# Optimization experiments

Hardware: AMD Instinct MI355X
Metric: run time of the kernel (lower is better)

## Reference

```python
import jax, jax.numpy as jnp
import numpy as np

B, C, H, W = 8, 384, 32, 32
HEADS = 12


def _relative_position_index(h, w):
    coords_h = np.arange(h)
    coords_w = np.arange(w)
    coords = np.stack(np.meshgrid(coords_h, coords_w, indexing='ij'))  # [2,h,w]
    flat = coords.reshape(2, -1)  # [2, N]
    rel = flat[:, :, None] - flat[:, None, :]  # [2, N, N]
    rel = rel.transpose(1, 2, 0)  # [N, N, 2]
    rel[:, :, 0] += h - 1
    rel[:, :, 1] += w - 1
    rel[:, :, 0] *= 2 * w - 1
    return rel.sum(-1).astype(np.int32)  # [N, N]


def setup_inputs() -> dict:
    key = jax.random.key(0)
    ks = jax.random.split(key, 6)
    std = 0.02
    x = jax.random.normal(ks[0], (B, C, H, W), dtype=jnp.float32)
    q_w = jax.random.normal(ks[1], (C, C), dtype=jnp.float32) * std
    q_b = jnp.zeros((C,), dtype=jnp.float32)
    kv_w = jax.random.normal(ks[2], (2 * C, C), dtype=jnp.float32) * std
    kv_b = jnp.zeros((2 * C,), dtype=jnp.float32)
    proj_w = jax.random.normal(ks[3], (C, C), dtype=jnp.float32) * std
    proj_b = jnp.zeros((C,), dtype=jnp.float32)
    n_table = (2 * H - 1) * (2 * W - 1)
    rpb_table = jax.random.normal(ks[4], (n_table, HEADS), dtype=jnp.float32) * std
    rel_index = jnp.asarray(_relative_position_index(H, W))  # [N, N] int32
    return {"x": x, "q_w": q_w, "q_b": q_b, "kv_w": kv_w, "kv_b": kv_b,
            "proj_w": proj_w, "proj_b": proj_b, "rpb_table": rpb_table,
            "rel_index": rel_index}


def reference(x, q_w, q_b, kv_w, kv_b, proj_w, proj_b, rpb_table, rel_index):
    b, c, h, w = x.shape
    n = h * w
    heads = rpb_table.shape[-1]
    hd = c // heads
    scale = hd ** (-0.5)

    xf = x.reshape(b, c, n)  # 1x1 conv == per-pixel matmul
    q = jnp.einsum('dc,bcn->bdn', q_w, xf) + q_b[:, None]
    q = q.reshape(b, heads, hd, n).transpose(0, 1, 3, 2)  # [b,h,n,hd]
    kv = jnp.einsum('dc,bcn->bdn', kv_w, xf) + kv_b[:, None]
    kv = kv.reshape(b, 2, heads, hd, n)
    k = kv[:, 0].transpose(0, 1, 3, 2)  # [b,h,n,hd]
    v = kv[:, 1].transpose(0, 1, 3, 2)

    attn = jnp.einsum('bhnd,bhmd->bhnm', q, k) * scale  # [b,h,n,n]
    bias = rpb_table[rel_index.reshape(-1)].reshape(n, n, heads)
    bias = bias.transpose(2, 0, 1)  # [h,n,n]
    attn = jax.nn.softmax(attn + bias[None], axis=-1)

    out = jnp.einsum('bhnm,bhmd->bhnd', attn, v)
    out = out.transpose(0, 1, 3, 2).reshape(b, c, h, w)
    out = jnp.einsum('dc,bchw->bdhw', proj_w, out) + proj_b[None, :, None, None]
    return out
```

## Files before the change

### kernel.cpp

```cpp
#include <hip/hip_runtime.h>
#include <hip/hip_bf16.h>

#define B_  8
#define C_  384
#define N_  1024
#define NH_ 12
#define HD_ 32
#define D3_ 1152

typedef __bf16 bf16x8 __attribute__((ext_vector_type(8)));
typedef __bf16 bf16x2 __attribute__((ext_vector_type(2)));
typedef float  f32x4  __attribute__((ext_vector_type(4)));

typedef const __attribute__((address_space(1))) unsigned int guint;
typedef __attribute__((address_space(3))) unsigned int luint;

__device__ __forceinline__ float b2f(ushort u) {
    return __uint_as_float(((unsigned int)u) << 16);
}
__device__ __forceinline__ ushort f2b(float f) {
    unsigned int i = __float_as_uint(f);
    unsigned int r = i + 0x7fffu + ((i >> 16) & 1u);
    return (ushort)(r >> 16);
}
__device__ __forceinline__ unsigned pk2(float a, float b) {
#if __has_builtin(__builtin_amdgcn_cvt_pk_bf16_f32)
    bf16x2 t = __builtin_amdgcn_cvt_pk_bf16_f32(a, b);
    return __builtin_bit_cast(unsigned, t);
#else
    return (unsigned)f2b(a) | ((unsigned)f2b(b) << 16);
#endif
}

#if __has_builtin(__builtin_amdgcn_exp2f)
#define EXP2 __builtin_amdgcn_exp2f
#else
#define EXP2 exp2f
#endif

__device__ __forceinline__ void gl2lds16(const void* g, void* l) {
    __builtin_amdgcn_global_load_lds((guint*)g, (luint*)l, 16, 0, 0);
}

#define C1_ 0.25505654204433796f
#define C2_ 1.4426950408889634f
#define TS_ 3972

__global__ __launch_bounds__(256) void setup(
    const float* __restrict__ x, const float* __restrict__ q_w,
    const float* __restrict__ kv_w, const float* __restrict__ proj_w,
    const float* __restrict__ q_b, const float* __restrict__ kv_b,
    const float* __restrict__ tab,
    ushort* __restrict__ xT, float* __restrict__ tabT,
    ushort* __restrict__ Wall, ushort* __restrict__ PW,
    float* __restrict__ ballf)
{
    __shared__ ushort T[64 * 72];
    const int bx = blockIdx.x, tid = threadIdx.x;

    if (bx < 768) {
        int t = bx;
        int nx = t & 15, cy = (t >> 4) % 6, b = t / 96;
        int n0 = nx * 64, c0 = cy * 64;
        {
            int i = tid >> 2;
            int ns = (tid & 3) * 16;
            const float* src = x + ((size_t)b * C_ + c0 + i) * N_ + n0 + ns;
            #pragma unroll
            for (int k4 = 0; k4 < 4; ++k4) {
                float4 f = *(const float4*)(src + k4 * 4);
                T[(ns + k4 * 4 + 0) * 72 + i] = f2b(f.x);
                T[(ns + k4 * 4 + 1) * 72 + i] = f2b(f.y);
                T[(ns + k4 * 4 + 2) * 72 + i] = f2b(f.z);
                T[(ns + k4 * 4 + 3) * 72 + i] = f2b(f.w);
            }
        }
        __syncthreads();
        {
            int j = tid >> 2;
            int cs = (tid & 3) * 16;
            ushort* dst = xT + ((size_t)b * N_ + n0 + j) * C_ + c0 + cs;
            *(uint4*)dst       = *(const uint4*)&T[j * 72 + cs];
            *(uint4*)(dst + 8) = *(const uint4*)&T[j * 72 + cs + 8];
        }
    } else if (bx < 1346) {
        const int NW4 = 110592, NP4 = 36864, NB4 = 288;
        int t = (bx - 768) * 256 + tid;
        if (t < NW4) {
            int e = t * 4;
            float4 f = (e < 147456) ? *(const float4*)(q_w + e)
                                    : *(const float4*)(kv_w + e - 147456);
            union { uint2 u; ushort s[4]; } o;
            o.u.x = pk2(f.x, f.y); o.u.y = pk2(f.z, f.w);
            *(uint2*)(Wall + e) = o.u;
        } else if (t < NW4 + NP4) {
            int e = (t - NW4) * 4;
            float4 f = *(const float4*)(proj_w + e);
            union { uint2 u; ushort s[4]; } o;
            o.u.x = pk2(f.x, f.y); o.u.y = pk2(f.z, f.w);
            *(uint2*)(PW + e) = o.u;
        } else if (t < NW4 + NP4 + NB4) {
            int e = (t - NW4 - NP4) * 4;
            float4 f = (e < 384) ? *(const float4*)(q_b + e)
                                 : *(const float4*)(kv_b + e - 384);
            *(float4*)(ballf + e) = f;
        }
    } else {
        int h = bx - 1346;
        for (int i = tid; i < 3969; i += 256)
            tabT[h * TS_ + i] = tab[(size_t)(3968 - i) * NH_ + h] * C2_;
        if (tid < 3) tabT[h * TS_ + 3969 + tid] = 0.0f;
    }
}

__global__ __launch_bounds__(256) void qkv_gemm5(
    const ushort* __restrict__ xT, const ushort* __restrict__ Wall,
    const float* __restrict__ ballf, ushort* __restrict__ Qt,
    ushort* __restrict__ Kt, ushort* __restrict__ Vtc)
{
    const int b = blockIdx.z, n0 = blockIdx.x * 128, d0 = blockIdx.y * 128;
    __shared__ ushort As[128 * 32];
    __shared__ ushort Bs[128 * 32];
    const int tid = threadIdx.x;
    const int lane = tid & 63, wave = tid >> 6;
    const int quad = lane >> 4, l16 = lane & 15;
    const int wn = (wave & 1) * 64, wd = (wave >> 1) * 64;

    f32x4 acc[4][4] = {};
    const ushort* xb = xT + ((size_t)b * N_ + n0) * C_;
    const ushort* wb = Wall + (size_t)d0 * C_;
    const int rowA = wave * 16 + (lane >> 2);
    const int fstage = ((lane >> 2) ^ (lane >> 4)) & 3;
    const int coff = ((lane & 3) ^ fstage) * 8;
    const int fread = ((l16 & 3) ^ ((l16 >> 2) & 3));
    const bool isV = (d0 >= 768);

    for (int c0 = 0; c0 < C_; c0 += 32) {
        #pragma unroll
        for (int k = 0; k < 2; ++k) {
            gl2lds16(xb + (size_t)(k * 64 + rowA) * C_ + c0 + coff,
                     &As[(size_t)(k * 256 + wave * 64) * 8]);
            gl2lds16(wb + (size_t)(k * 64 + rowA) * C_ + c0 + coff,
                     &Bs[(size_t)(k * 256 + wave * 64) * 8]);
        }
        __syncthreads();
        bf16x8 af[4], bfr[4];
        #pragma unroll
        for (int i = 0; i < 4; ++i)
            af[i] = *(const bf16x8*)&As[(wn + i * 16 + l16) * 32 + (quad ^ fread) * 8];
        #pragma unroll
        for (int j = 0; j < 4; ++j)
            bfr[j] = *(const bf16x8*)&Bs[(wd + j * 16 + l16) * 32 + (quad ^ fread) * 8];
        if (!isV) {
            #pragma unroll
            for (int i = 0; i < 4; ++i)
                #pragma unroll
                for (int j = 0; j < 4; ++j)
                    acc[i][j] = __builtin_amdgcn_mfma_f32_16x16x32_bf16(bfr[i], af[j], acc[i][j], 0, 0, 0);
        } else {
            #pragma unroll
            for (int i = 0; i < 4; ++i)
                #pragma unroll
                for (int j = 0; j < 4; ++j)
                    acc[i][j] = __builtin_amdgcn_mfma_f32_16x16x32_bf16(af[i], bfr[j], acc[i][j], 0, 0, 0);
        }
        __syncthreads();
    }

    if (!isV) {
        ushort* dst = (d0 < 384) ? Qt : Kt;
        const float sc = (d0 < 384) ? C1_ : 1.0f;
        const int reg0 = (d0 < 384) ? 0 : 384;
        #pragma unroll
        for (int i = 0; i < 4; ++i) {
            int dloc = wd + i * 16;
            int dg = d0 - reg0 + dloc;
            int h = dg >> 5;
            int dc = (dg & 31) + quad * 4;
            float4 bvv = *(const float4*)(ballf + d0 + dloc + quad * 4);
            size_t hb = (size_t)(b * NH_ + h) * N_;
            #pragma unroll
            for (int j = 0; j < 4; ++j) {
                int n = n0 + wn + j * 16 + l16;
                uint2 w;
                w.x = pk2((acc[i][j][0] + bvv.x) * sc, (acc[i][j][1] + bvv.y) * sc);
                w.y = pk2((acc[i][j][2] + bvv.z) * sc, (acc[i][j][3] + bvv.w) * sc);
                *(uint2*)(dst + (hb + n) * 32 + dc) = w;
            }
        }
    } else {
        #pragma unroll
        for (int j = 0; j < 4; ++j) {
            int dloc = wd + j * 16 + l16;
            int vd = d0 - 768 + dloc;
            int h = vd >> 5, dc = vd & 31;
            float bv = ballf[d0 + dloc];
            size_t hbase = (size_t)(b * NH_ + h) * 32768 + dc * 32;
            #pragma unroll
            for (int i = 0; i < 4; ++i) {
                int n = n0 + wn + i * 16 + quad * 4;
                size_t cbase = hbase + (size_t)((n >> 5)) * 1024 + (n & 31);
                uint2 w;
                w.x = pk2(acc[i][j][0] + bv, acc[i][j][1] + bv);
                w.y = pk2(acc[i][j][2] + bv, acc[i][j][3] + bv);
                *(uint2*)(Vtc + cbase) = w;
            }
        }
    }
}

__global__ __launch_bounds__(256, 4) void attn6(
    const ushort* __restrict__ Qt, const ushort* __restrict__ Kt,
    const ushort* __restrict__ Vtc, const float* __restrict__ tabT,
    ushort* __restrict__ O)
{
    const int bid = blockIdx.x;
    const int bh96 = bid % 96;
    const int nx = bid / 96;
    const int b = bh96 / 12, h = bh96 % 12;

    __shared__ float tabL[TS_];
    __shared__ ushort Pa[4096];

    const int tid = threadIdx.x;
    const int lane = tid & 63, wave = tid >> 6;
    const int quad = lane >> 4, l16 = lane & 15;
    const int bh = b * NH_ + h;

    {
        const float* th = tabT + h * TS_;
        int i = tid * 4;
        #pragma unroll
        for (int k = 0; k < 4; ++k) {
            if (i < TS_) *(float4*)&tabL[i] = *(const float4*)&th[i];
            i += 1024;
        }
    }
    __syncthreads();

    const int qs = nx * 4 + wave;
    const int q = qs * 16 + l16;
    const ushort* Kbh = Kt + (size_t)bh * N_ * 32;
    const ushort* Vbh = Vtc + (size_t)bh * 16 * 2048;

    bf16x8 qf = *(const bf16x8*)(Qt + ((size_t)bh * N_ + q) * 32 + quad * 8);
    const int ibx = (31 - (q >> 5)) * 63 + (31 - (q & 31));

    bf16x8 ones;
    #pragma unroll
    for (int j = 0; j < 8; ++j) ones[j] = (__bf16)1.0f;

    f32x4 oacc0 = {}, oacc1 = {}, lacc = {};

    ushort* Pw = &Pa[wave * 1024];
    const int pswz = l16 & 0xE;
    const int pwr = l16 * 64;

    const ushort* kp0 = Kbh + l16 * 32 + quad * 8;
    bf16x8 ka0 = *(const bf16x8*)(kp0);
    bf16x8 ka1 = *(const bf16x8*)(kp0 + 512);
    bf16x8 ka2 = *(const bf16x8*)(kp0 + 1024);
    bf16x8 ka3 = *(const bf16x8*)(kp0 + 1536);

    for (int mc = 0; mc < 16; ++mc) {
        const ushort* vp = Vbh + mc * 2048 + l16 * 32 + quad * 8;
        bf16x8 va00 = *(const bf16x8*)(vp);
        bf16x8 va01 = *(const bf16x8*)(vp + 512);
        bf16x8 va10 = *(const bf16x8*)(vp + 1024);
        bf16x8 va11 = *(const bf16x8*)(vp + 1536);
        const ushort* kn = Kbh + ((mc + 1) & 15) * 2048 + l16 * 32 + quad * 8;
        bf16x8 kb0 = *(const bf16x8*)(kn);
        bf16x8 kb1 = *(const bf16x8*)(kn + 512);
        bf16x8 kb2 = *(const bf16x8*)(kn + 1024);
        bf16x8 kb3 = *(const bf16x8*)(kn + 1536);

        const float* Tb = tabL + ibx + mc * 126 + quad * 4;
        f32x4 cb0, cb1, cb2, cb3;
        #pragma unroll
        for (int e = 0; e < 4; ++e) {
            cb0[e] = Tb[e];
            cb1[e] = Tb[e + 16];
            cb2[e] = Tb[e + 63];
            cb3[e] = Tb[e + 79];
        }

        f32x4 s0 = __builtin_amdgcn_mfma_f32_16x16x32_bf16(ka0, qf, cb0, 0, 0, 0);
        f32x4 s1 = __builtin_amdgcn_mfma_f32_16x16x32_bf16(ka1, qf, cb1, 0, 0, 0);
        f32x4 s2 = __builtin_amdgcn_mfma_f32_16x16x32_bf16(ka2, qf, cb2, 0, 0, 0);
        f32x4 s3 = __builtin_amdgcn_mfma_f32_16x16x32_bf16(ka3, qf, cb3, 0, 0, 0);
        ka0 = kb0; ka1 = kb1; ka2 = kb2; ka3 = kb3;

        {
            uint2 w;
            w.x = pk2(EXP2(s0[0]), EXP2(s0[1]));
            w.y = pk2(EXP2(s0[2]), EXP2(s0[3]));
            *(uint2*)(Pw + pwr + (((0 + quad) ^ pswz) * 4)) = w;
            w.x = pk2(EXP2(s1[0]), EXP2(s1[1]));
            w.y = pk2(EXP2(s1[2]), EXP2(s1[3]));
            *(uint2*)(Pw + pwr + (((4 + quad) ^ pswz) * 4)) = w;
            w.x = pk2(EXP2(s2[0]), EXP2(s2[1]));
            w.y = pk2(EXP2(s2[2]), EXP2(s2[3]));
            *(uint2*)(Pw + pwr + (((8 + quad) ^ pswz) * 4)) = w;
            w.x = pk2(EXP2(s3[0]), EXP2(s3[1]));
            w.y = pk2(EXP2(s3[2]), EXP2(s3[3]));
            *(uint2*)(Pw + pwr + (((12 + quad) ^ pswz) * 4)) = w;
        }

        bf16x8 pb0 = *(const bf16x8*)(Pw + pwr + (((quad * 2) ^ pswz) * 4));
        lacc  = __builtin_amdgcn_mfma_f32_16x16x32_bf16(ones, pb0, lacc, 0, 0, 0);
        oacc0 = __builtin_amdgcn_mfma_f32_16x16x32_bf16(va00, pb0, oacc0, 0, 0, 0);
        oacc1 = __builtin_amdgcn_mfma_f32_16x16x32_bf16(va01, pb0, oacc1, 0, 0, 0);
        bf16x8 pb1 = *(const bf16x8*)(Pw + pwr + (((8 + quad * 2) ^ pswz) * 4));
        lacc  = __builtin_amdgcn_mfma_f32_16x16x32_bf16(ones, pb1, lacc, 0, 0, 0);
        oacc0 = __builtin_amdgcn_mfma_f32_16x16x32_bf16(va10, pb1, oacc0, 0, 0, 0);
        oacc1 = __builtin_amdgcn_mfma_f32_16x16x32_bf16(va11, pb1, oacc1, 0, 0, 0);
    }

    float inv = 1.0f / lacc[0];

    ushort* ob = O + ((size_t)(b * N_ + q)) * C_ + h * HD_;
    uint2 w0, w1;
    w0.x = pk2(oacc0[0] * inv, oacc0[1] * inv);
    w0.y = pk2(oacc0[2] * inv, oacc0[3] * inv);
    *(uint2*)(ob + quad * 4) = w0;
    w1.x = pk2(oacc1[0] * inv, oacc1[1] * inv);
    w1.y = pk2(oacc1[2] * inv, oacc1[3] * inv);
    *(uint2*)(ob + 16 + quad * 4) = w1;
}

__global__ __launch_bounds__(256) void proj_gemm3(
    const ushort* __restrict__ O, const ushort* __restrict__ PW,
    const float* __restrict__ pb, float* __restrict__ out)
{
    const int b = blockIdx.z, n0 = blockIdx.x * 128, d0 = blockIdx.y * 128;
    __shared__ ushort As[128 * 32];
    __shared__ ushort Bs[128 * 32];
    const int tid = threadIdx.x;
    const int lane = tid & 63, wave = tid >> 6;
    const int quad = lane >> 4, l16 = lane & 15;
    const int wa = (wave & 1) * 64, wb = (wave >> 1) * 64;

    f32x4 acc[4][4] = {};
    const ushort* ab = PW + (size_t)d0 * C_;
    const ushort* bbp = O + ((size_t)b * N_ + n0) * C_;
    const int rowA = wave * 16 + (lane >> 2);
    const int fstage = ((lane >> 2) ^ (lane >> 4)) & 3;
    const int coff = ((lane & 3) ^ fstage) * 8;
    const int fread = ((l16 & 3) ^ ((l16 >> 2) & 3));

    for (int c0 = 0; c0 < C_; c0 += 32) {
        #pragma unroll
        for (int k = 0; k < 2; ++k) {
            gl2lds16(ab + (size_t)(k * 64 + rowA) * C_ + c0 + coff,
                     &As[(size_t)(k * 256 + wave * 64) * 8]);
            gl2lds16(bbp + (size_t)(k * 64 + rowA) * C_ + c0 + coff,
                     &Bs[(size_t)(k * 256 + wave * 64) * 8]);
        }
        __syncthreads();
        bf16x8 af[4], bfr[4];
        #pragma unroll
        for (int i = 0; i < 4; ++i)
            af[i] = *(const bf16x8*)&As[(wa + i * 16 + l16) * 32 + (quad ^ fread) * 8];
        #pragma unroll
        for (int j = 0; j < 4; ++j)
            bfr[j] = *(const bf16x8*)&Bs[(wb + j * 16 + l16) * 32 + (quad ^ fread) * 8];
        #pragma unroll
        for (int i = 0; i < 4; ++i)
            #pragma unroll
            for (int j = 0; j < 4; ++j)
                acc[i][j] = __builtin_amdgcn_mfma_f32_16x16x32_bf16(af[i], bfr[j], acc[i][j], 0, 0, 0);
        __syncthreads();
    }

    #pragma unroll
    for (int i = 0; i < 4; ++i) {
        #pragma unroll
        for (int r = 0; r < 4; ++r) {
            int d = d0 + wa + i * 16 + quad * 4 + r;
            float bv = pb[d];
            float* op = out + ((size_t)b * C_ + d) * N_ + n0 + wb;
            #pragma unroll
            for (int j = 0; j < 4; ++j)
                op[j * 16 + l16] = acc[i][j][r] + bv;
        }
    }
}

extern "C" void kernel_launch(void* const* d_in, const int* in_sizes, int n_in,
                              void* d_out, int out_size, void* d_ws, size_t ws_size,
                              hipStream_t stream)
{
    const float* x      = (const float*)d_in[0];
    const float* q_w    = (const float*)d_in[1];
    const float* q_b    = (const float*)d_in[2];
    const float* kv_w   = (const float*)d_in[3];
    const float* kv_b   = (const float*)d_in[4];
    const float* proj_w = (const float*)d_in[5];
    const float* proj_b = (const float*)d_in[6];
    const float* rpb    = (const float*)d_in[7];
    float* out = (float*)d_out;

    char* ws = (char*)d_ws;
    ushort* xT    = (ushort*)(ws);
    ushort* Qt    = (ushort*)(ws +  6291456);
    ushort* Kt    = (ushort*)(ws + 12582912);
    ushort* Vtc   = (ushort*)(ws + 18874368);
    ushort* O     = (ushort*)(ws + 25165824);
    float*  tabT  = (float*) (ws + 31457280);
    ushort* Wall  = (ushort*)(ws + 31647936);
    ushort* PW    = (ushort*)(ws + 32532672);
    float*  ballf = (float*) (ws + 32827584);

    setup      <<<dim3(1358), 256, 0, stream>>>(x, q_w, kv_w, proj_w, q_b, kv_b, rpb,
                                                xT, tabT, Wall, PW, ballf);
    qkv_gemm5  <<<dim3(8, 9, B_), 256, 0, stream>>>(xT, Wall, ballf, Qt, Kt, Vtc);
    attn6      <<<dim3(1536), 256, 0, stream>>>(Qt, Kt, Vtc, tabT, O);
    proj_gemm3 <<<dim3(8, 3, B_), 256, 0, stream>>>(O, PW, proj_b, out);
}
```

Before: 168.9 us.

## Process four query strips per wave in attention and halve projection GEMM tile height

The attention kernel now runs 2 waves per block, and each wave handles 4 query strips of 16 rows against the same K/V fragments. Each K and V load is therefore reused across four query tiles instead of one, which cuts global and L2 traffic per unit of work. In exchange, register pressure goes up (four sets of accumulators) and there are half as many blocks. The projection GEMM tile is reduced from 128 to 64 output channels, doubling the grid to 384 blocks for better CU fill at lower per-block reuse.

New measurement: 158.1 us. -6.4%, faster.

```diff
diff --git a/kernel.cpp b/kernel.cpp
--- a/kernel.cpp
+++ b/kernel.cpp
@@ -209,7 +209,7 @@
     }
 }
 
-__global__ __launch_bounds__(256, 4) void attn6(
+__global__ __launch_bounds__(128) void attn7(
     const ushort* __restrict__ Qt, const ushort* __restrict__ Kt,
     const ushort* __restrict__ Vtc, const float* __restrict__ tabT,
     ushort* __restrict__ O)
@@ -220,7 +220,7 @@
     const int b = bh96 / 12, h = bh96 % 12;
 
     __shared__ float tabL[TS_];
-    __shared__ ushort Pa[4096];
+    __shared__ ushort Pa[8192];
 
     const int tid = threadIdx.x;
     const int lane = tid & 63, wave = tid >> 6;
@@ -229,33 +229,37 @@
 
     {
         const float* th = tabT + h * TS_;
-        int i = tid * 4;
-        #pragma unroll
-        for (int k = 0; k < 4; ++k) {
-            if (i < TS_) *(float4*)&tabL[i] = *(const float4*)&th[i];
-            i += 1024;
-        }
+        for (int i = tid * 4; i < TS_; i += 512)
+            *(float4*)&tabL[i] = *(const float4*)&th[i];
     }
     __syncthreads();
 
-    const int qs = nx * 4 + wave;
-    const int q = qs * 16 + l16;
+    const int qs0 = nx * 8 + wave * 4;
     const ushort* Kbh = Kt + (size_t)bh * N_ * 32;
     const ushort* Vbh = Vtc + (size_t)bh * 16 * 2048;
 
-    bf16x8 qf = *(const bf16x8*)(Qt + ((size_t)bh * N_ + q) * 32 + quad * 8);
-    const int ibx = (31 - (q >> 5)) * 63 + (31 - (q & 31));
+    bf16x8 qf[4];
+    int ib[4];
+    #pragma unroll
+    for (int st = 0; st < 4; ++st) {
+        int q = (qs0 + st) * 16 + l16;
+        qf[st] = *(const bf16x8*)(Qt + ((size_t)bh * N_ + q) * 32 + quad * 8);
+        ib[st] = (31 - (q >> 5)) * 63 + (31 - (q & 31));
+    }
 
     bf16x8 ones;
     #pragma unroll
     for (int j = 0; j < 8; ++j) ones[j] = (__bf16)1.0f;
 
-    f32x4 oacc0 = {}, oacc1 = {}, lacc = {};
-
-    ushort* Pw = &Pa[wave * 1024];
+    f32x4 oacc[4][2] = {};
+    f32x4 lacc[4] = {};
+
+    ushort* PwW = &Pa[wave * 4096];
     const int pswz = l16 & 0xE;
     const int pwr = l16 * 64;
 
+    {
+    }
     const ushort* kp0 = Kbh + l16 * 32 + quad * 8;
     bf16x8 ka0 = *(const bf16x8*)(kp0);
     bf16x8 ka1 = *(const bf16x8*)(kp0 + 512);
@@ -274,73 +278,83 @@
         bf16x8 kb2 = *(const bf16x8*)(kn + 1024);
         bf16x8 kb3 = *(const bf16x8*)(kn + 1536);
 
-        const float* Tb = tabL + ibx + mc * 126 + quad * 4;
-        f32x4 cb0, cb1, cb2, cb3;
-        #pragma unroll
-        for (int e = 0; e < 4; ++e) {
-            cb0[e] = Tb[e];
-            cb1[e] = Tb[e + 16];
-            cb2[e] = Tb[e + 63];
-            cb3[e] = Tb[e + 79];
-        }
-
-        f32x4 s0 = __builtin_amdgcn_mfma_f32_16x16x32_bf16(ka0, qf, cb0, 0, 0, 0);
-        f32x4 s1 = __builtin_amdgcn_mfma_f32_16x16x32_bf16(ka1, qf, cb1, 0, 0, 0);
-        f32x4 s2 = __builtin_amdgcn_mfma_f32_16x16x32_bf16(ka2, qf, cb2, 0, 0, 0);
-        f32x4 s3 = __builtin_amdgcn_mfma_f32_16x16x32_bf16(ka3, qf, cb3, 0, 0, 0);
+        #pragma unroll
+        for (int sp = 0; sp < 2; ++sp) {
+            f32x4 s[2][4];
+            #pragma unroll
+            for (int u = 0; u < 2; ++u) {
+                const int st = sp * 2 + u;
+                const float* Tb = tabL + ib[st] + mc * 126 + quad * 4;
+                f32x4 cb0, cb1, cb2, cb3;
+                #pragma unroll
+                for (int e = 0; e < 4; ++e) {
+                    cb0[e] = Tb[e];
+                    cb1[e] = Tb[e + 16];
+                    cb2[e] = Tb[e + 63];
+                    cb3[e] = Tb[e + 79];
+                }
+                s[u][0] = __builtin_amdgcn_mfma_f32_16x16x32_bf16(ka0, qf[st], cb0, 0, 0, 0);
+                s[u][1] = __builtin_amdgcn_mfma_f32_16x16x32_bf16(ka1, qf[st], cb1, 0, 0, 0);
+                s[u][2] = __builtin_amdgcn_mfma_f32_16x16x32_bf16(ka2, qf[st], cb2, 0, 0, 0);
+                s[u][3] = __builtin_amdgcn_mfma_f32_16x16x32_bf16(ka3, qf[st], cb3, 0, 0, 0);
+            }
+            #pragma unroll
+            for (int u = 0; u < 2; ++u) {
+                const int st = sp * 2 + u;
+                ushort* Pw = PwW + st * 1024;
+                #pragma unroll
+                for (int t = 0; t < 4; ++t) {
+                    uint2 w;
+                    w.x = pk2(EXP2(s[u][t][0]), EXP2(s[u][t][1]));
+                    w.y = pk2(EXP2(s[u][t][2]), EXP2(s[u][t][3]));
+                    *(uint2*)(Pw + pwr + (((t * 4 + quad) ^ pswz) * 4)) = w;
+                }
+            }
+            #pragma unroll
+            for (int u = 0; u < 2; ++u) {
+                const int st = sp * 2 + u;
+                ushort* Pw = PwW + st * 1024;
+                bf16x8 pb0 = *(const bf16x8*)(Pw + pwr + (((quad * 2) ^ pswz) * 4));
+                lacc[st]    = __builtin_amdgcn_mfma_f32_16x16x32_bf16(ones, pb0, lacc[st], 0, 0, 0);
+                oacc[st][0] = __builtin_amdgcn_mfma_f32_16x16x32_bf16(va00, pb0, oacc[st][0], 0, 0, 0);
+                oacc[st][1] = __builtin_amdgcn_mfma_f32_16x16x32_bf16(va01, pb0, oacc[st][1], 0, 0, 0);
+                bf16x8 pb1 = *(const bf16x8*)(Pw + pwr + (((8 + quad * 2) ^ pswz) * 4));
+                lacc[st]    = __builtin_amdgcn_mfma_f32_16x16x32_bf16(ones, pb1, lacc[st], 0, 0, 0);
+                oacc[st][0] = __builtin_amdgcn_mfma_f32_16x16x32_bf16(va10, pb1, oacc[st][0], 0, 0, 0);
+                oacc[st][1] = __builtin_amdgcn_mfma_f32_16x16x32_bf16(va11, pb1, oacc[st][1], 0, 0, 0);
+            }
+        }
         ka0 = kb0; ka1 = kb1; ka2 = kb2; ka3 = kb3;
-
-        {
-            uint2 w;
-            w.x = pk2(EXP2(s0[0]), EXP2(s0[1]));
-            w.y = pk2(EXP2(s0[2]), EXP2(s0[3]));
-            *(uint2*)(Pw + pwr + (((0 + quad) ^ pswz) * 4)) = w;
-            w.x = pk2(EXP2(s1[0]), EXP2(s1[1]));
-            w.y = pk2(EXP2(s1[2]), EXP2(s1[3]));
-            *(uint2*)(Pw + pwr + (((4 + quad) ^ pswz) * 4)) = w;
-            w.x = pk2(EXP2(s2[0]), EXP2(s2[1]));
-            w.y = pk2(EXP2(s2[2]), EXP2(s2[3]));
-            *(uint2*)(Pw + pwr + (((8 + quad) ^ pswz) * 4)) = w;
-            w.x = pk2(EXP2(s3[0]), EXP2(s3[1]));
-            w.y = pk2(EXP2(s3[2]), EXP2(s3[3]));
-            *(uint2*)(Pw + pwr + (((12 + quad) ^ pswz) * 4)) = w;
-        }
-
-        bf16x8 pb0 = *(const bf16x8*)(Pw + pwr + (((quad * 2) ^ pswz) * 4));
-        lacc  = __builtin_amdgcn_mfma_f32_16x16x32_bf16(ones, pb0, lacc, 0, 0, 0);
-        oacc0 = __builtin_amdgcn_mfma_f32_16x16x32_bf16(va00, pb0, oacc0, 0, 0, 0);
-        oacc1 = __builtin_amdgcn_mfma_f32_16x16x32_bf16(va01, pb0, oacc1, 0, 0, 0);
-        bf16x8 pb1 = *(const bf16x8*)(Pw + pwr + (((8 + quad * 2) ^ pswz) * 4));
-        lacc  = __builtin_amdgcn_mfma_f32_16x16x32_bf16(ones, pb1, lacc, 0, 0, 0);
-        oacc0 = __builtin_amdgcn_mfma_f32_16x16x32_bf16(va10, pb1, oacc0, 0, 0, 0);
-        oacc1 = __builtin_amdgcn_mfma_f32_16x16x32_bf16(va11, pb1, oacc1, 0, 0, 0);
-    }
-
-    float inv = 1.0f / lacc[0];
-
-    ushort* ob = O + ((size_t)(b * N_ + q)) * C_ + h * HD_;
-    uint2 w0, w1;
-    w0.x = pk2(oacc0[0] * inv, oacc0[1] * inv);
-    w0.y = pk2(oacc0[2] * inv, oacc0[3] * inv);
-    *(uint2*)(ob + quad * 4) = w0;
-    w1.x = pk2(oacc1[0] * inv, oacc1[1] * inv);
-    w1.y = pk2(oacc1[2] * inv, oacc1[3] * inv);
-    *(uint2*)(ob + 16 + quad * 4) = w1;
-}
-
-__global__ __launch_bounds__(256) void proj_gemm3(
+    }
+
+    #pragma unroll
+    for (int st = 0; st < 4; ++st) {
+        float inv = 1.0f / lacc[st][0];
+        int q = (qs0 + st) * 16 + l16;
+        ushort* ob = O + ((size_t)(b * N_ + q)) * C_ + h * HD_;
+        uint2 w0, w1;
+        w0.x = pk2(oacc[st][0][0] * inv, oacc[st][0][1] * inv);
+        w0.y = pk2(oacc[st][0][2] * inv, oacc[st][0][3] * inv);
+        *(uint2*)(ob + quad * 4) = w0;
+        w1.x = pk2(oacc[st][1][0] * inv, oacc[st][1][1] * inv);
+        w1.y = pk2(oacc[st][1][2] * inv, oacc[st][1][3] * inv);
+        *(uint2*)(ob + 16 + quad * 4) = w1;
+    }
+}
+
+__global__ __launch_bounds__(256) void proj_gemm4(
     const ushort* __restrict__ O, const ushort* __restrict__ PW,
     const float* __restrict__ pb, float* __restrict__ out)
 {
-    const int b = blockIdx.z, n0 = blockIdx.x * 128, d0 = blockIdx.y * 128;
-    __shared__ ushort As[128 * 32];
+    const int b = blockIdx.z, n0 = blockIdx.x * 128, d0 = blockIdx.y * 64;
+    __shared__ ushort As[64 * 32];
     __shared__ ushort Bs[128 * 32];
     const int tid = threadIdx.x;
     const int lane = tid & 63, wave = tid >> 6;
     const int quad = lane >> 4, l16 = lane & 15;
-    const int wa = (wave & 1) * 64, wb = (wave >> 1) * 64;
-
-    f32x4 acc[4][4] = {};
+    const int wd = (wave & 1) * 32, wn = (wave >> 1) * 64;
+
+    f32x4 acc[2][4] = {};
     const ushort* ab = PW + (size_t)d0 * C_;
     const ushort* bbp = O + ((size_t)b * N_ + n0) * C_;
     const int rowA = wave * 16 + (lane >> 2);
@@ -349,23 +363,21 @@
     const int fread = ((l16 & 3) ^ ((l16 >> 2) & 3));
 
     for (int c0 = 0; c0 < C_; c0 += 32) {
-        #pragma unroll
-        for (int k = 0; k < 2; ++k) {
-            gl2lds16(ab + (size_t)(k * 64 + rowA) * C_ + c0 + coff,
-                     &As[(size_t)(k * 256 + wave * 64) * 8]);
+        gl2lds16(ab + (size_t)rowA * C_ + c0 + coff, &As[(size_t)(wave * 64) * 8]);
+        #pragma unroll
+        for (int k = 0; k < 2; ++k)
             gl2lds16(bbp + (size_t)(k * 64 + rowA) * C_ + c0 + coff,
                      &Bs[(size_t)(k * 256 + wave * 64) * 8]);
-        }
         __syncthreads();
-        bf16x8 af[4], bfr[4];
-        #pragma unroll
-        for (int i = 0; i < 4; ++i)
-            af[i] = *(const bf16x8*)&As[(wa + i * 16 + l16) * 32 + (quad ^ fread) * 8];
+        bf16x8 af[2], bfr[4];
+        #pragma unroll
+        for (int i = 0; i < 2; ++i)
+            af[i] = *(const bf16x8*)&As[(wd + i * 16 + l16) * 32 + (quad ^ fread) * 8];
         #pragma unroll
         for (int j = 0; j < 4; ++j)
-            bfr[j] = *(const bf16x8*)&Bs[(wb + j * 16 + l16) * 32 + (quad ^ fread) * 8];
-        #pragma unroll
-        for (int i = 0; i < 4; ++i)
+            bfr[j] = *(const bf16x8*)&Bs[(wn + j * 16 + l16) * 32 + (quad ^ fread) * 8];
+        #pragma unroll
+        for (int i = 0; i < 2; ++i)
             #pragma unroll
             for (int j = 0; j < 4; ++j)
                 acc[i][j] = __builtin_amdgcn_mfma_f32_16x16x32_bf16(af[i], bfr[j], acc[i][j], 0, 0, 0);
@@ -373,12 +385,12 @@
     }
 
     #pragma unroll
-    for (int i = 0; i < 4; ++i) {
+    for (int i = 0; i < 2; ++i) {
         #pragma unroll
         for (int r = 0; r < 4; ++r) {
-            int d = d0 + wa + i * 16 + quad * 4 + r;
+            int d = d0 + wd + i * 16 + quad * 4 + r;
             float bv = pb[d];
-            float* op = out + ((size_t)b * C_ + d) * N_ + n0 + wb;
+            float* op = out + ((size_t)b * C_ + d) * N_ + n0 + wn;
             #pragma unroll
             for (int j = 0; j < 4; ++j)
                 op[j * 16 + l16] = acc[i][j][r] + bv;
@@ -414,6 +426,6 @@
     setup      <<<dim3(1358), 256, 0, stream>>>(x, q_w, kv_w, proj_w, q_b, kv_b, rpb,
                                                 xT, tabT, Wall, PW, ballf);
     qkv_gemm5  <<<dim3(8, 9, B_), 256, 0, stream>>>(xT, Wall, ballf, Qt, Kt, Vtc);
-    attn6      <<<dim3(1536), 256, 0, stream>>>(Qt, Kt, Vtc, tabT, O);
-    proj_gemm3 <<<dim3(8, 3, B_), 256, 0, stream>>>(O, PW, proj_b, out);
-}
+    attn7      <<<dim3(768), 128, 0, stream>>>(Qt, Kt, Vtc, tabT, O);
+    proj_gemm4 <<<dim3(8, 6, B_), 256, 0, stream>>>(O, PW, proj_b, out);
+}
```

## Split attention key range across wave pairs and process two query strips per wave

Applied to the files above, without the earlier changes.

The attention kernel now has each wave handle two 16-query strips while covering only half of the key/value range. The two halves are merged through shared memory before normalisation and the bf16 store. Each K/V fragment loaded from global memory is reused across two query strips, so per-wave global traffic for K and V is halved. In exchange it adds an extra sync and LDS reduction, doubles the shared P buffer, drops the occupancy hint from launch_bounds, and raises register pressure from the doubled accumulators.

After: 154.4 us. 1.09x faster.

```diff
diff --git a/kernel.cpp b/kernel.cpp
--- a/kernel.cpp
+++ b/kernel.cpp
@@ -209,7 +209,7 @@
     }
 }
 
-__global__ __launch_bounds__(256, 4) void attn6(
+__global__ __launch_bounds__(256) void attn8(
     const ushort* __restrict__ Qt, const ushort* __restrict__ Kt,
     const ushort* __restrict__ Vtc, const float* __restrict__ tabT,
     ushort* __restrict__ O)
@@ -220,49 +220,54 @@
     const int b = bh96 / 12, h = bh96 % 12;
 
     __shared__ float tabL[TS_];
-    __shared__ ushort Pa[4096];
+    __shared__ ushort Pa[8192];
 
     const int tid = threadIdx.x;
     const int lane = tid & 63, wave = tid >> 6;
     const int quad = lane >> 4, l16 = lane & 15;
+    const int sp = wave >> 1;
+    const int mh = wave & 1;
     const int bh = b * NH_ + h;
 
     {
         const float* th = tabT + h * TS_;
-        int i = tid * 4;
-        #pragma unroll
-        for (int k = 0; k < 4; ++k) {
-            if (i < TS_) *(float4*)&tabL[i] = *(const float4*)&th[i];
-            i += 1024;
-        }
+        for (int i = tid * 4; i < TS_; i += 1024)
+            *(float4*)&tabL[i] = *(const float4*)&th[i];
     }
     __syncthreads();
 
-    const int qs = nx * 4 + wave;
-    const int q = qs * 16 + l16;
+    const int qs0 = nx * 4 + sp * 2;
     const ushort* Kbh = Kt + (size_t)bh * N_ * 32;
     const ushort* Vbh = Vtc + (size_t)bh * 16 * 2048;
 
-    bf16x8 qf = *(const bf16x8*)(Qt + ((size_t)bh * N_ + q) * 32 + quad * 8);
-    const int ibx = (31 - (q >> 5)) * 63 + (31 - (q & 31));
+    bf16x8 qf[2];
+    int ib[2];
+    #pragma unroll
+    for (int st = 0; st < 2; ++st) {
+        int q = (qs0 + st) * 16 + l16;
+        qf[st] = *(const bf16x8*)(Qt + ((size_t)bh * N_ + q) * 32 + quad * 8);
+        ib[st] = (31 - (q >> 5)) * 63 + (31 - (q & 31));
+    }
 
     bf16x8 ones;
     #pragma unroll
     for (int j = 0; j < 8; ++j) ones[j] = (__bf16)1.0f;
 
-    f32x4 oacc0 = {}, oacc1 = {}, lacc = {};
-
-    ushort* Pw = &Pa[wave * 1024];
+    f32x4 oacc[2][2] = {};
+    f32x4 lacc[2] = {};
+
+    ushort* Pw0 = &Pa[wave * 2048];
     const int pswz = l16 & 0xE;
     const int pwr = l16 * 64;
 
-    const ushort* kp0 = Kbh + l16 * 32 + quad * 8;
+    const int mc0 = mh * 8;
+    const ushort* kp0 = Kbh + mc0 * 2048 + l16 * 32 + quad * 8;
     bf16x8 ka0 = *(const bf16x8*)(kp0);
     bf16x8 ka1 = *(const bf16x8*)(kp0 + 512);
     bf16x8 ka2 = *(const bf16x8*)(kp0 + 1024);
     bf16x8 ka3 = *(const bf16x8*)(kp0 + 1536);
 
-    for (int mc = 0; mc < 16; ++mc) {
+    for (int mc = mc0; mc < mc0 + 8; ++mc) {
         const ushort* vp = Vbh + mc * 2048 + l16 * 32 + quad * 8;
         bf16x8 va00 = *(const bf16x8*)(vp);
         bf16x8 va01 = *(const bf16x8*)(vp + 512);
@@ -274,23 +279,23 @@
         bf16x8 kb2 = *(const bf16x8*)(kn + 1024);
         bf16x8 kb3 = *(const bf16x8*)(kn + 1536);
 
-        const float* Tb = tabL + ibx + mc * 126 + quad * 4;
-        f32x4 cb0, cb1, cb2, cb3;
-        #pragma unroll
-        for (int e = 0; e < 4; ++e) {
-            cb0[e] = Tb[e];
-            cb1[e] = Tb[e + 16];
-            cb2[e] = Tb[e + 63];
-            cb3[e] = Tb[e + 79];
-        }
-
-        f32x4 s0 = __builtin_amdgcn_mfma_f32_16x16x32_bf16(ka0, qf, cb0, 0, 0, 0);
-        f32x4 s1 = __builtin_amdgcn_mfma_f32_16x16x32_bf16(ka1, qf, cb1, 0, 0, 0);
-        f32x4 s2 = __builtin_amdgcn_mfma_f32_16x16x32_bf16(ka2, qf, cb2, 0, 0, 0);
-        f32x4 s3 = __builtin_amdgcn_mfma_f32_16x16x32_bf16(ka3, qf, cb3, 0, 0, 0);
-        ka0 = kb0; ka1 = kb1; ka2 = kb2; ka3 = kb3;
-
-        {
+        #pragma unroll
+        for (int st = 0; st < 2; ++st) {
+            const float* Tb = tabL + ib[st] + mc * 126 + quad * 4;
+            f32x4 cb0, cb1, cb2, cb3;
+            #pragma unroll
+            for (int e = 0; e < 4; ++e) {
+                cb0[e] = Tb[e];
+                cb1[e] = Tb[e + 16];
+                cb2[e] = Tb[e + 63];
+                cb3[e] = Tb[e + 79];
+            }
+            f32x4 s0 = __builtin_amdgcn_mfma_f32_16x16x32_bf16(ka0, qf[st], cb0, 0, 0, 0);
+            f32x4 s1 = __builtin_amdgcn_mfma_f32_16x16x32_bf16(ka1, qf[st], cb1, 0, 0, 0);
+            f32x4 s2 = __builtin_amdgcn_mfma_f32_16x16x32_bf16(ka2, qf[st], cb2, 0, 0, 0);
+            f32x4 s3 = __builtin_amdgcn_mfma_f32_16x16x32_bf16(ka3, qf[st], cb3, 0, 0, 0);
+
+            ushort* Pw = Pw0 + st * 1024;
             uint2 w;
             w.x = pk2(EXP2(s0[0]), EXP2(s0[1]));
             w.y = pk2(EXP2(s0[2]), EXP2(s0[3]));
@@ -304,28 +309,53 @@
             w.x = pk2(EXP2(s3[0]), EXP2(s3[1]));
             w.y = pk2(EXP2(s3[2]), EXP2(s3[3]));
             *(uint2*)(Pw + pwr + (((12 + quad) ^ pswz) * 4)) = w;
-        }
-
-        bf16x8 pb0 = *(const bf16x8*)(Pw + pwr + (((quad * 2) ^ pswz) * 4));
-        lacc  = __builtin_amdgcn_mfma_f32_16x16x32_bf16(ones, pb0, lacc, 0, 0, 0);
-        oacc0 = __builtin_amdgcn_mfma_f32_16x16x32_bf16(va00, pb0, oacc0, 0, 0, 0);
-        oacc1 = __builtin_amdgcn_mfma_f32_16x16x32_bf16(va01, pb0, oacc1, 0, 0, 0);
-        bf16x8 pb1 = *(const bf16x8*)(Pw + pwr + (((8 + quad * 2) ^ pswz) * 4));
-        lacc  = __builtin_amdgcn_mfma_f32_16x16x32_bf16(ones, pb1, lacc, 0, 0, 0);
-        oacc0 = __builtin_amdgcn_mfma_f32_16x16x32_bf16(va10, pb1, oacc0, 0, 0, 0);
-        oacc1 = __builtin_amdgcn_mfma_f32_16x16x32_bf16(va11, pb1, oacc1, 0, 0, 0);
-    }
-
-    float inv = 1.0f / lacc[0];
-
-    ushort* ob = O + ((size_t)(b * N_ + q)) * C_ + h * HD_;
-    uint2 w0, w1;
-    w0.x = pk2(oacc0[0] * inv, oacc0[1] * inv);
-    w0.y = pk2(oacc0[2] * inv, oacc0[3] * inv);
-    *(uint2*)(ob + quad * 4) = w0;
-    w1.x = pk2(oacc1[0] * inv, oacc1[1] * inv);
-    w1.y = pk2(oacc1[2] * inv, oacc1[3] * inv);
-    *(uint2*)(ob + 16 + quad * 4) = w1;
+
+            bf16x8 pb0 = *(const bf16x8*)(Pw + pwr + (((quad * 2) ^ pswz) * 4));
+            lacc[st]    = __builtin_amdgcn_mfma_f32_16x16x32_bf16(ones, pb0, lacc[st], 0, 0, 0);
+            oacc[st][0] = __builtin_amdgcn_mfma_f32_16x16x32_bf16(va00, pb0, oacc[st][0], 0, 0, 0);
+            oacc[st][1] = __builtin_amdgcn_mfma_f32_16x16x32_bf16(va01, pb0, oacc[st][1], 0, 0, 0);
+            bf16x8 pb1 = *(const bf16x8*)(Pw + pwr + (((8 + quad * 2) ^ pswz) * 4));
+            lacc[st]    = __builtin_amdgcn_mfma_f32_16x16x32_bf16(ones, pb1, lacc[st], 0, 0, 0);
+            oacc[st][0] = __builtin_amdgcn_mfma_f32_16x16x32_bf16(va10, pb1, oacc[st][0], 0, 0, 0);
+            oacc[st][1] = __builtin_amdgcn_mfma_f32_16x16x32_bf16(va11, pb1, oacc[st][1], 0, 0, 0);
+        }
+        ka0 = kb0; ka1 = kb1; ka2 = kb2; ka3 = kb3;
+    }
+
+    __syncthreads();
+    float* M = (float*)Pa;
+    if (mh) {
+        #pragma unroll
+        for (int st = 0; st < 2; ++st) {
+            #pragma unroll
+            for (int dt = 0; dt < 2; ++dt)
+                #pragma unroll
+                for (int e = 0; e < 4; ++e)
+                    M[(sp * 18 + st * 8 + dt * 4 + e) * 64 + lane] = oacc[st][dt][e];
+            M[(sp * 18 + 16 + st) * 64 + lane] = lacc[st][0];
+        }
+    }
+    __syncthreads();
+    if (!mh) {
+        #pragma unroll
+        for (int st = 0; st < 2; ++st) {
+            float l = lacc[st][0] + M[(sp * 18 + 16 + st) * 64 + lane];
+            float inv = 1.0f / l;
+            int q = (qs0 + st) * 16 + l16;
+            ushort* ob = O + ((size_t)(b * N_ + q)) * C_ + h * HD_;
+            #pragma unroll
+            for (int dt = 0; dt < 2; ++dt) {
+                float v0 = oacc[st][dt][0] + M[(sp * 18 + st * 8 + dt * 4 + 0) * 64 + lane];
+                float v1 = oacc[st][dt][1] + M[(sp * 18 + st * 8 + dt * 4 + 1) * 64 + lane];
+                float v2 = oacc[st][dt][2] + M[(sp * 18 + st * 8 + dt * 4 + 2) * 64 + lane];
+                float v3 = oacc[st][dt][3] + M[(sp * 18 + st * 8 + dt * 4 + 3) * 64 + lane];
+                uint2 w;
+                w.x = pk2(v0 * inv, v1 * inv);
+                w.y = pk2(v2 * inv, v3 * inv);
+                *(uint2*)(ob + dt * 16 + quad * 4) = w;
+            }
+        }
+    }
 }
 
 __global__ __launch_bounds__(256) void proj_gemm3(
@@ -414,6 +444,6 @@
     setup      <<<dim3(1358), 256, 0, stream>>>(x, q_w, kv_w, proj_w, q_b, kv_b, rpb,
                                                 xT, tabT, Wall, PW, ballf);
     qkv_gemm5  <<<dim3(8, 9, B_), 256, 0, stream>>>(xT, Wall, ballf, Qt, Kt, Vtc);
-    attn6      <<<dim3(1536), 256, 0, stream>>>(Qt, Kt, Vtc, tabT, O);
+    attn8      <<<dim3(1536), 256, 0, stream>>>(Qt, Kt, Vtc, tabT, O);
     proj_gemm3 <<<dim3(8, 3, B_), 256, 0, stream>>>(O, PW, proj_b, out);
 }
```
